# Performance work log

Measured on AMD Instinct MI355X. Metric: run time of the kernel, lower is better.

The kernel has to match this reference:

```python
import jax, jax.numpy as jnp
import numpy as np

N_NODES = 50000


def gcn_conv(x, edge_index, W, b, num_nodes):
    """PyG GCNConv: add self-loops, symmetric norm, gather-scatter aggregate."""
    h = x @ W  # [N, out]
    row = jnp.concatenate([edge_index[0], jnp.arange(num_nodes)])  # sources (+ self loops)
    col = jnp.concatenate([edge_index[1], jnp.arange(num_nodes)])  # targets
    deg = jax.ops.segment_sum(jnp.ones_like(col, dtype=h.dtype), col, num_segments=num_nodes)
    dinv = jnp.where(deg > 0, jax.lax.rsqrt(deg), 0.0)
    norm = dinv[row] * dinv[col]  # [E+N]
    msgs = h[row] * norm[:, None]  # gather + scale
    out = jax.ops.segment_sum(msgs, col, num_segments=num_nodes)  # scatter-add
    return out + b


def setup_inputs() -> dict:
    key = jax.random.key(0)
    ks = jax.random.split(key, 8)
    F_in, H, D = 50, 50, 64
    E_train, Ep, En = 1600000, 200000, 200000
    x = jax.random.normal(ks[0], (N_NODES, F_in), dtype=jnp.float32)
    train_pos_edge_index = jax.random.randint(ks[1], (2, E_train), 0, N_NODES)
    pos_edge_index = jax.random.randint(ks[2], (2, Ep), 0, N_NODES)
    neg_edge_index = jax.random.randint(ks[3], (2, En), 0, N_NODES)
    # Glorot-ish params for the two GCN layers
    W1 = jax.random.normal(ks[4], (F_in, H), dtype=jnp.float32) * (1.0 / np.sqrt(F_in))
    b1 = jnp.zeros((H,), dtype=jnp.float32)
    W2 = jax.random.normal(ks[5], (H, D), dtype=jnp.float32) * (1.0 / np.sqrt(H))
    b2 = jnp.zeros((D,), dtype=jnp.float32)
    return {"x": x, "train_pos_edge_index": train_pos_edge_index,
            "pos_edge_index": pos_edge_index, "neg_edge_index": neg_edge_index,
            "W1": W1, "b1": b1, "W2": W2, "b2": b2}


def reference(x, train_pos_edge_index, pos_edge_index, neg_edge_index, W1, b1, W2, b2):
    # encode: conv1 -> relu -> conv2
    h = gcn_conv(x, train_pos_edge_index, W1, b1, N_NODES)
    h = jax.nn.relu(h)
    z = gcn_conv(h, train_pos_edge_index, W2, b2, N_NODES)  # [N, D]
    # decode: dot product over concatenated pos/neg edge endpoints
    edge_index = jnp.concatenate([pos_edge_index, neg_edge_index], axis=-1)
    logits = jnp.sum(z[edge_index[0]] * z[edge_index[1]], axis=-1)  # [Ep+En]
    return logits
```

## Files before the change

### kernel.cpp

```cpp
#include <hip/hip_runtime.h>
#include <hip/hip_bf16.h>
#include <hip/hip_fp16.h>


constexpr int N_NODES = 50000;
constexpr int NBITS = 6;
constexpr int BNODES = 1 << NBITS;
constexpr int NBUCK = (N_NODES + BNODES - 1) / BNODES;
constexpr int CAP = 2560;
constexpr int CHUNK = 2048;
constexpr int NTILE = 4;
constexpr int TROWS = 12500;

union H4 {
    uint2 u;
    __half2 h[2];
};

__device__ inline float4 h4_to_f4(H4 a) {
    float2 f0 = __half22float2(a.h[0]);
    float2 f1 = __half22float2(a.h[1]);
    return make_float4(f0.x, f0.y, f1.x, f1.y);
}

__device__ inline H4 f4_to_h4(float4 v) {
    H4 r;
    r.h[0] = __floats2half2_rn(v.x, v.y);
    r.h[1] = __floats2half2_rn(v.z, v.w);
    return r;
}

__device__ inline void unpack16(uint4 w0, uint4 w1, int* r) {
    r[0] = (int)(w0.x & 0xffffu);  r[1] = (int)(w0.x >> 16);
    r[2] = (int)(w0.y & 0xffffu);  r[3] = (int)(w0.y >> 16);
    r[4] = (int)(w0.z & 0xffffu);  r[5] = (int)(w0.z >> 16);
    r[6] = (int)(w0.w & 0xffffu);  r[7] = (int)(w0.w >> 16);
    r[8] = (int)(w1.x & 0xffffu);  r[9] = (int)(w1.x >> 16);
    r[10] = (int)(w1.y & 0xffffu); r[11] = (int)(w1.y >> 16);
    r[12] = (int)(w1.z & 0xffffu); r[13] = (int)(w1.z >> 16);
    r[14] = (int)(w1.w & 0xffffu); r[15] = (int)(w1.w >> 16);
}

__global__ __launch_bounds__(256) void partition_kernel(const int4* __restrict__ row4,
                                                        const int4* __restrict__ col4, int E,
                                                        int* __restrict__ cursor,
                                                        unsigned* __restrict__ bEdges) {
    __shared__ unsigned ed[CHUNK];
    __shared__ int cnt[NBUCK];
    __shared__ int base[NBUCK];
    int t = threadIdx.x;
    int e0 = blockIdx.x * CHUNK;
    int n = min(CHUNK, E - e0);
    int n4 = n >> 2;
    for (int i = t; i < NBUCK; i += 256) cnt[i] = 0;
    __syncthreads();
    const int4* r4 = row4 + (e0 >> 2);
    const int4* c4 = col4 + (e0 >> 2);
    for (int i = t; i < n4; i += 256) {
        int4 r = r4[i];
        int4 c = c4[i];
        ed[i * 4 + 0] = ((unsigned)r.x << 16) | (unsigned)c.x;
        ed[i * 4 + 1] = ((unsigned)r.y << 16) | (unsigned)c.y;
        ed[i * 4 + 2] = ((unsigned)r.z << 16) | (unsigned)c.z;
        ed[i * 4 + 3] = ((unsigned)r.w << 16) | (unsigned)c.w;
        atomicAdd(&cnt[c.x >> NBITS], 1);
        atomicAdd(&cnt[c.y >> NBITS], 1);
        atomicAdd(&cnt[c.z >> NBITS], 1);
        atomicAdd(&cnt[c.w >> NBITS], 1);
    }
    __syncthreads();
    for (int i = t; i < NBUCK; i += 256) base[i] = cnt[i] ? atomicAdd(&cursor[i], cnt[i]) : 0;
    __syncthreads();
    for (int i = t; i < NBUCK; i += 256) cnt[i] = 0;
    __syncthreads();
    for (int i = t; i < n; i += 256) {
        unsigned p = ed[i];
        int bk = (int)(p & 0xffffu) >> NBITS;
        int pos = base[bk] + atomicAdd(&cnt[bk], 1);
        if (pos < CAP) bEdges[(size_t)bk * CAP + pos] = p;
    }
}

__global__ __launch_bounds__(256) void bucket_csr_kernel(const int* __restrict__ cursor,
                                                         const unsigned* __restrict__ bEdges,
                                                         unsigned short* __restrict__ srcIdx,
                                                         unsigned* __restrict__ rowmeta,
                                                         float* __restrict__ dinv, int N) {
    __shared__ unsigned ed[CAP];
    __shared__ unsigned short srcL[CAP];
    __shared__ int tdeg[BNODES * NTILE];
    __shared__ int toff[BNODES * NTILE];
    __shared__ int totPad;
    int b = blockIdx.x;
    int tx = threadIdx.x;
    int cnt = min(cursor[b], CAP);
    for (int i = tx; i < BNODES * NTILE; i += 256) tdeg[i] = 0;
    for (int i = tx; i < CAP; i += 256) srcL[i] = 0;
    __syncthreads();
    const unsigned* seg = bEdges + (size_t)b * CAP;
    for (int i = tx; i < cnt; i += 256) {
        unsigned p = seg[i];
        ed[i] = p;
        int l = p & (BNODES - 1);
        int tl = (int)(p >> 16) / TROWS;
        atomicAdd(&tdeg[l * NTILE + tl], 1);
    }
    __syncthreads();
    if (tx < BNODES) {
        int s0 = tdeg[tx * NTILE + 0];
        int s1 = tdeg[tx * NTILE + 1];
        int s2 = tdeg[tx * NTILE + 2];
        int s3 = tdeg[tx * NTILE + 3];
        int d = s0 + s1 + s2 + s3;
        int dpad = (d + 7) & ~7;
        int s = dpad;
#pragma unroll
        for (int off = 1; off < BNODES; off <<= 1) {
            int o = __shfl_up(s, off, 64);
            if (tx >= off) s += o;
        }
        int ex = s - dpad;
        toff[tx * NTILE + 0] = ex;
        toff[tx * NTILE + 1] = ex + s0;
        toff[tx * NTILE + 2] = ex + s0 + s1;
        toff[tx * NTILE + 3] = ex + s0 + s1 + s2;
        if (tx == 63) totPad = min(s, CAP);
        int node = b * BNODES + tx;
        if (node < N) {
            unsigned st = (unsigned)(b * CAP + ex);
            rowmeta[node] = (st << 7) | (unsigned)d;
            dinv[node] = rsqrtf((float)d + 1.0f);
        }
    }
    __syncthreads();
    for (int i = tx; i < BNODES * NTILE; i += 256) tdeg[i] = 0;
    __syncthreads();
    for (int i = tx; i < cnt; i += 256) {
        unsigned p = ed[i];
        int l = p & (BNODES - 1);
        int tl = (int)(p >> 16) / TROWS;
        int pos = toff[l * NTILE + tl] + atomicAdd(&tdeg[l * NTILE + tl], 1);
        srcL[pos] = (unsigned short)(p >> 16);
    }
    __syncthreads();
    int tot = totPad;
    for (int i = tx; i < tot; i += 256) srcIdx[(size_t)b * CAP + i] = srcL[i];
}

template <typename TIN, int K, int INS, int MV>
__global__ __launch_bounds__(256) void matmul_scale_kernel(const TIN* __restrict__ X,
                                                           const float* __restrict__ W,
                                                           const float* __restrict__ dinv,
                                                           uint2* __restrict__ Hs, int N) {
    __shared__ float4 Ws4[K * 16];
    for (int i = threadIdx.x; i < K * 64; i += 256) {
        int k = i >> 6;
        int c = i & 63;
        ((float*)Ws4)[i] = (c < MV) ? W[k * MV + c] : 0.f;
    }
    __syncthreads();
    int tid = blockIdx.x * blockDim.x + threadIdx.x;
    int row = tid >> 4;
    int q = tid & 15;
    if (row >= N) return;
    const TIN* xr = X + (size_t)row * INS;
    float4 acc = make_float4(0.f, 0.f, 0.f, 0.f);
#pragma unroll
    for (int k = 0; k < K; ++k) {
        float xv = (float)xr[k];
        float4 w = Ws4[k * 16 + q];
        acc.x = fmaf(xv, w.x, acc.x);
        acc.y = fmaf(xv, w.y, acc.y);
        acc.z = fmaf(xv, w.z, acc.z);
        acc.w = fmaf(xv, w.w, acc.w);
    }
    float d = dinv[row];
    acc.x *= d;
    acc.y *= d;
    acc.z *= d;
    acc.w *= d;
    Hs[(size_t)row * 16 + q] = f4_to_h4(acc).u;
}

__device__ inline float4 gather_sum(const unsigned short* __restrict__ srcIdx,
                                    const uint2* __restrict__ hs, int node, int q,
                                    unsigned meta) {
    int start = (int)(meta >> 7);
    int d = (int)(meta & 127u);
    int end = start + d;
    H4 t;
    t.u = hs[(size_t)node * 16 + q];
    float4 acc = h4_to_f4(t);
    int j = start;
    while (j + 16 <= end) {
        const uint4* ip = (const uint4*)(srcIdx + j);
        int r[16];
        unpack16(ip[0], ip[1], r);
#pragma unroll
        for (int u = 0; u < 16; ++u) {
            H4 hv;
            hv.u = hs[(size_t)r[u] * 16 + q];
            float4 a = h4_to_f4(hv);
            acc.x += a.x;
            acc.y += a.y;
            acc.z += a.z;
            acc.w += a.w;
        }
        j += 16;
    }
    if (j < end) {
        const uint4* ip = (const uint4*)(srcIdx + j);
        int r[16];
        unpack16(ip[0], ip[1], r);
#pragma unroll
        for (int u = 0; u < 16; ++u) {
            float m = (j + u < end) ? 1.f : 0.f;
            H4 hv;
            hv.u = hs[(size_t)r[u] * 16 + q];
            float4 a = h4_to_f4(hv);
            acc.x = fmaf(m, a.x, acc.x);
            acc.y = fmaf(m, a.y, acc.y);
            acc.z = fmaf(m, a.z, acc.z);
            acc.w = fmaf(m, a.w, acc.w);
        }
    }
    return acc;
}

template <int BC>
__global__ __launch_bounds__(256) void agg_mm_kernel(const unsigned* __restrict__ rowmeta,
                                                     const unsigned short* __restrict__ srcIdx,
                                                     const uint2* __restrict__ hs,
                                                     const float* __restrict__ dinv,
                                                     const float* __restrict__ b1,
                                                     const float* __restrict__ W2,
                                                     uint2* __restrict__ out, int N) {
    __shared__ float4 Ws4[50 * 16];
    __shared__ float h1s[16][68];
    for (int i = threadIdx.x; i < 50 * 64; i += 256) ((float*)Ws4)[i] = W2[i];
    __syncthreads();
    int tid = blockIdx.x * blockDim.x + threadIdx.x;
    int node = tid >> 4;
    int q = tid & 15;
    int g = threadIdx.x >> 4;
    float4 acc = gather_sum(srcIdx, hs, node, q, rowmeta[node]);
    float dv = dinv[node];
    int f = q * 4;
    float4 h1;
    h1.x = fmaxf(dv * acc.x + (f + 0 < BC ? b1[f + 0] : 0.f), 0.f);
    h1.y = fmaxf(dv * acc.y + (f + 1 < BC ? b1[f + 1] : 0.f), 0.f);
    h1.z = fmaxf(dv * acc.z + (f + 2 < BC ? b1[f + 2] : 0.f), 0.f);
    h1.w = fmaxf(dv * acc.w + (f + 3 < BC ? b1[f + 3] : 0.f), 0.f);
    h1s[g][f + 0] = h1.x;
    h1s[g][f + 1] = h1.y;
    h1s[g][f + 2] = h1.z;
    h1s[g][f + 3] = h1.w;
    __syncthreads();
    float4 a2 = make_float4(0.f, 0.f, 0.f, 0.f);
#pragma unroll
    for (int k = 0; k < 50; ++k) {
        float xv = h1s[g][k];
        float4 w = Ws4[k * 16 + q];
        a2.x = fmaf(xv, w.x, a2.x);
        a2.y = fmaf(xv, w.y, a2.y);
        a2.z = fmaf(xv, w.z, a2.z);
        a2.w = fmaf(xv, w.w, a2.w);
    }
    a2.x *= dv;
    a2.y *= dv;
    a2.z *= dv;
    a2.w *= dv;
    out[(size_t)node * 16 + q] = f4_to_h4(a2).u;
}

template <int BC>
__global__ __launch_bounds__(256) void agg_kernel(const unsigned* __restrict__ rowmeta,
                                                  const unsigned short* __restrict__ srcIdx,
                                                  const uint2* __restrict__ hs,
                                                  const float* __restrict__ dinv,
                                                  const float* __restrict__ b,
                                                  uint2* __restrict__ out, int N) {
    int tid = blockIdx.x * blockDim.x + threadIdx.x;
    int node = tid >> 4;
    int q = tid & 15;
    if (node >= N) return;
    float4 acc = gather_sum(srcIdx, hs, node, q, rowmeta[node]);
    float dv = dinv[node];
    int f = q * 4;
    float4 v;
    v.x = dv * acc.x + (f + 0 < BC ? b[f + 0] : 0.f);
    v.y = dv * acc.y + (f + 1 < BC ? b[f + 1] : 0.f);
    v.z = dv * acc.z + (f + 2 < BC ? b[f + 2] : 0.f);
    v.w = dv * acc.w + (f + 3 < BC ? b[f + 3] : 0.f);
    out[(size_t)node * 16 + q] = f4_to_h4(v).u;
}

__global__ __launch_bounds__(256) void decode_kernel(const int* __restrict__ pos,
                                                     const int* __restrict__ neg, int Ep, int En,
                                                     const uint2* __restrict__ z,
                                                     float* __restrict__ logits) {
    int tid = blockIdx.x * blockDim.x + threadIdx.x;
    int e = tid >> 4;
    int q = tid & 15;
    int Etot = Ep + En;
    if (e >= Etot) return;
    int a, bn;
    if (e < Ep) {
        a = pos[e];
        bn = pos[Ep + e];
    } else {
        int t = e - Ep;
        a = neg[t];
        bn = neg[En + t];
    }
    H4 ha, hb;
    ha.u = z[(size_t)a * 16 + q];
    hb.u = z[(size_t)bn * 16 + q];
    float4 za = h4_to_f4(ha);
    float4 zb = h4_to_f4(hb);
    float v = za.x * zb.x + za.y * zb.y + za.z * zb.z + za.w * zb.w;
    v += __shfl_xor(v, 1, 64);
    v += __shfl_xor(v, 2, 64);
    v += __shfl_xor(v, 4, 64);
    v += __shfl_xor(v, 8, 64);
    if (q == 0) logits[e] = v;
}

extern "C" void kernel_launch(void* const* d_in, const int* in_sizes, int n_in,
                              void* d_out, int out_size, void* d_ws, size_t ws_size,
                              hipStream_t stream) {
    const float* x = (const float*)d_in[0];
    const int* train = (const int*)d_in[1];
    const int* pos = (const int*)d_in[2];
    const int* neg = (const int*)d_in[3];
    const float* W1 = (const float*)d_in[4];
    const float* b1 = (const float*)d_in[5];
    const float* W2 = (const float*)d_in[6];
    const float* b2 = (const float*)d_in[7];
    float* logits = (float*)d_out;

    const int FIN = 50;
    const int N = in_sizes[0] / FIN;
    const int E = in_sizes[1] / 2;
    const int Ep = in_sizes[2] / 2;
    const int En = in_sizes[3] / 2;

    const int* t_row = train;
    const int* t_col = train + E;

    float* dinv = (float*)d_ws;
    __half* buf0 = (__half*)(dinv + N);
    __half* buf1 = buf0 + (size_t)N * 64;
    unsigned* rowmeta = (unsigned*)(buf1 + (size_t)N * 64);
    int* cursor = (int*)(rowmeta + N);
    uintptr_t sp = (uintptr_t)(cursor + NBUCK);
    sp = (sp + 15) & ~(uintptr_t)15;
    unsigned short* srcIdx = (unsigned short*)sp;
    unsigned* bEdges = (unsigned*)buf0;

    hipMemsetAsync(cursor, 0, (size_t)NBUCK * sizeof(int), stream);

    partition_kernel<<<(E + CHUNK - 1) / CHUNK, 256, 0, stream>>>((const int4*)t_row,
                                                                  (const int4*)t_col, E, cursor,
                                                                  bEdges);
    bucket_csr_kernel<<<NBUCK, 256, 0, stream>>>(cursor, bEdges, srcIdx, rowmeta, dinv, N);

    const int MMB = (N * 16 + 255) / 256;

    matmul_scale_kernel<float, 50, 50, 50><<<MMB, 256, 0, stream>>>(x, W1, dinv, (uint2*)buf0, N);
    agg_mm_kernel<50><<<MMB, 256, 0, stream>>>(rowmeta, srcIdx, (const uint2*)buf0, dinv, b1, W2,
                                               (uint2*)buf1, N);
    agg_kernel<64><<<MMB, 256, 0, stream>>>(rowmeta, srcIdx, (const uint2*)buf1, dinv, b2,
                                            (uint2*)buf0, N);
    decode_kernel<<<((Ep + En) * 16 + 255) / 256, 256, 0, stream>>>(pos, neg, Ep, En,
                                                                    (const uint2*)buf0, logits);
}
```

Measured before the change: 224.4 us.

## Fuse layer-1 matmul into bucket CSR build and widen decode loads

Folds the first dense matmul (x@W1 scaled by dinv) into the bucket CSR kernel, so each 64-node bucket block stages its x rows and W1 in shared memory and writes Hs directly. This removes one kernel launch and the global re-read of dinv. bEdges moves to its own workspace region instead of aliasing buf0, because buf0 is now written in the same kernel that reads bEdges. The partition chunk size is doubled to 4096, and decode uses 8 lanes with 16-byte loads per edge instead of 16 lanes with 8-byte loads. The trade-off is more shared memory per block, which may lower occupancy, and only NBUCK (~782) blocks are available to do the matmul.

```diff
diff --git a/kernel.cpp b/kernel.cpp
--- a/kernel.cpp
+++ b/kernel.cpp
@@ -8,7 +8,7 @@
 constexpr int BNODES = 1 << NBITS;
 constexpr int NBUCK = (N_NODES + BNODES - 1) / BNODES;
 constexpr int CAP = 2560;
-constexpr int CHUNK = 2048;
+constexpr int CHUNK = 4096;
 constexpr int NTILE = 4;
 constexpr int TROWS = 12500;
 
@@ -39,6 +39,14 @@
     r[10] = (int)(w1.y & 0xffffu); r[11] = (int)(w1.y >> 16);
     r[12] = (int)(w1.z & 0xffffu); r[13] = (int)(w1.z >> 16);
     r[14] = (int)(w1.w & 0xffffu); r[15] = (int)(w1.w >> 16);
+}
+
+__device__ inline float hdot2(unsigned ua, unsigned ub) {
+    __half2 ha = *(__half2*)&ua;
+    __half2 hb = *(__half2*)&ub;
+    float2 fa = __half22float2(ha);
+    float2 fb = __half22float2(hb);
+    return fa.x * fb.x + fa.y * fb.y;
 }
 
 __global__ __launch_bounds__(256) void partition_kernel(const int4* __restrict__ row4,
@@ -81,16 +89,22 @@
     }
 }
 
-__global__ __launch_bounds__(256) void bucket_csr_kernel(const int* __restrict__ cursor,
-                                                         const unsigned* __restrict__ bEdges,
-                                                         unsigned short* __restrict__ srcIdx,
-                                                         unsigned* __restrict__ rowmeta,
-                                                         float* __restrict__ dinv, int N) {
+__global__ __launch_bounds__(256) void bucket_csr_mm_kernel(const int* __restrict__ cursor,
+                                                            const unsigned* __restrict__ bEdges,
+                                                            const float* __restrict__ x,
+                                                            const float* __restrict__ W1,
+                                                            unsigned short* __restrict__ srcIdx,
+                                                            unsigned* __restrict__ rowmeta,
+                                                            float* __restrict__ dinv,
+                                                            uint2* __restrict__ Hs, int N) {
     __shared__ unsigned ed[CAP];
     __shared__ unsigned short srcL[CAP];
     __shared__ int tdeg[BNODES * NTILE];
     __shared__ int toff[BNODES * NTILE];
     __shared__ int totPad;
+    __shared__ float dinvL[BNODES];
+    __shared__ float4 Ws4[50 * 16];
+    __shared__ float xs[BNODES][51];
     int b = blockIdx.x;
     int tx = threadIdx.x;
     int cnt = min(cursor[b], CAP);
@@ -104,6 +118,17 @@
         int l = p & (BNODES - 1);
         int tl = (int)(p >> 16) / TROWS;
         atomicAdd(&tdeg[l * NTILE + tl], 1);
+    }
+    for (int i = tx; i < 50 * 64; i += 256) {
+        int k = i >> 6;
+        int c = i & 63;
+        ((float*)Ws4)[i] = (c < 50) ? W1[k * 50 + c] : 0.f;
+    }
+    for (int i = tx; i < BNODES * 50; i += 256) {
+        int l = i / 50;
+        int k = i - l * 50;
+        int node = b * BNODES + l;
+        xs[l][k] = (node < N) ? x[(size_t)node * 50 + k] : 0.f;
     }
     __syncthreads();
     if (tx < BNODES) {
@@ -125,11 +150,13 @@
         toff[tx * NTILE + 2] = ex + s0 + s1;
         toff[tx * NTILE + 3] = ex + s0 + s1 + s2;
         if (tx == 63) totPad = min(s, CAP);
+        float dvv = rsqrtf((float)d + 1.0f);
+        dinvL[tx] = dvv;
         int node = b * BNODES + tx;
         if (node < N) {
             unsigned st = (unsigned)(b * CAP + ex);
             rowmeta[node] = (st << 7) | (unsigned)d;
-            dinv[node] = rsqrtf((float)d + 1.0f);
+            dinv[node] = dvv;
         }
     }
     __syncthreads();
@@ -145,41 +172,29 @@
     __syncthreads();
     int tot = totPad;
     for (int i = tx; i < tot; i += 256) srcIdx[(size_t)b * CAP + i] = srcL[i];
-}
-
-template <typename TIN, int K, int INS, int MV>
-__global__ __launch_bounds__(256) void matmul_scale_kernel(const TIN* __restrict__ X,
-                                                           const float* __restrict__ W,
-                                                           const float* __restrict__ dinv,
-                                                           uint2* __restrict__ Hs, int N) {
-    __shared__ float4 Ws4[K * 16];
-    for (int i = threadIdx.x; i < K * 64; i += 256) {
-        int k = i >> 6;
-        int c = i & 63;
-        ((float*)Ws4)[i] = (c < MV) ? W[k * MV + c] : 0.f;
-    }
-    __syncthreads();
-    int tid = blockIdx.x * blockDim.x + threadIdx.x;
-    int row = tid >> 4;
-    int q = tid & 15;
-    if (row >= N) return;
-    const TIN* xr = X + (size_t)row * INS;
-    float4 acc = make_float4(0.f, 0.f, 0.f, 0.f);
-#pragma unroll
-    for (int k = 0; k < K; ++k) {
-        float xv = (float)xr[k];
-        float4 w = Ws4[k * 16 + q];
-        acc.x = fmaf(xv, w.x, acc.x);
-        acc.y = fmaf(xv, w.y, acc.y);
-        acc.z = fmaf(xv, w.z, acc.z);
-        acc.w = fmaf(xv, w.w, acc.w);
-    }
-    float d = dinv[row];
-    acc.x *= d;
-    acc.y *= d;
-    acc.z *= d;
-    acc.w *= d;
-    Hs[(size_t)row * 16 + q] = f4_to_h4(acc).u;
+    int q = tx & 15;
+    int g = tx >> 4;
+#pragma unroll
+    for (int rep = 0; rep < 4; ++rep) {
+        int l = g + rep * 16;
+        float4 acc = make_float4(0.f, 0.f, 0.f, 0.f);
+#pragma unroll
+        for (int k = 0; k < 50; ++k) {
+            float xv = xs[l][k];
+            float4 w = Ws4[k * 16 + q];
+            acc.x = fmaf(xv, w.x, acc.x);
+            acc.y = fmaf(xv, w.y, acc.y);
+            acc.z = fmaf(xv, w.z, acc.z);
+            acc.w = fmaf(xv, w.w, acc.w);
+        }
+        float dv = dinvL[l];
+        acc.x *= dv;
+        acc.y *= dv;
+        acc.z *= dv;
+        acc.w *= dv;
+        int node = b * BNODES + l;
+        if (node < N) Hs[(size_t)node * 16 + q] = f4_to_h4(acc).u;
+    }
 }
 
 __device__ inline float4 gather_sum(const unsigned short* __restrict__ srcIdx,
@@ -297,11 +312,11 @@
 
 __global__ __launch_bounds__(256) void decode_kernel(const int* __restrict__ pos,
                                                      const int* __restrict__ neg, int Ep, int En,
-                                                     const uint2* __restrict__ z,
+                                                     const uint4* __restrict__ z4,
                                                      float* __restrict__ logits) {
     int tid = blockIdx.x * blockDim.x + threadIdx.x;
-    int e = tid >> 4;
-    int q = tid & 15;
+    int e = tid >> 3;
+    int q = tid & 7;
     int Etot = Ep + En;
     if (e >= Etot) return;
     int a, bn;
@@ -313,16 +328,12 @@
         a = neg[t];
         bn = neg[En + t];
     }
-    H4 ha, hb;
-    ha.u = z[(size_t)a * 16 + q];
-    hb.u = z[(size_t)bn * 16 + q];
-    float4 za = h4_to_f4(ha);
-    float4 zb = h4_to_f4(hb);
-    float v = za.x * zb.x + za.y * zb.y + za.z * zb.z + za.w * zb.w;
+    uint4 ua = z4[(size_t)a * 8 + q];
+    uint4 ub = z4[(size_t)bn * 8 + q];
+    float v = hdot2(ua.x, ub.x) + hdot2(ua.y, ub.y) + hdot2(ua.z, ub.z) + hdot2(ua.w, ub.w);
     v += __shfl_xor(v, 1, 64);
     v += __shfl_xor(v, 2, 64);
     v += __shfl_xor(v, 4, 64);
-    v += __shfl_xor(v, 8, 64);
     if (q == 0) logits[e] = v;
 }
 
@@ -356,22 +367,24 @@
     uintptr_t sp = (uintptr_t)(cursor + NBUCK);
     sp = (sp + 15) & ~(uintptr_t)15;
     unsigned short* srcIdx = (unsigned short*)sp;
-    unsigned* bEdges = (unsigned*)buf0;
+    uintptr_t bp = (uintptr_t)(srcIdx + (size_t)NBUCK * CAP);
+    bp = (bp + 15) & ~(uintptr_t)15;
+    unsigned* bEdges = (unsigned*)bp;
 
     hipMemsetAsync(cursor, 0, (size_t)NBUCK * sizeof(int), stream);
 
     partition_kernel<<<(E + CHUNK - 1) / CHUNK, 256, 0, stream>>>((const int4*)t_row,
                                                                   (const int4*)t_col, E, cursor,
                                                                   bEdges);
-    bucket_csr_kernel<<<NBUCK, 256, 0, stream>>>(cursor, bEdges, srcIdx, rowmeta, dinv, N);
+    bucket_csr_mm_kernel<<<NBUCK, 256, 0, stream>>>(cursor, bEdges, x, W1, srcIdx, rowmeta, dinv,
+                                                    (uint2*)buf0, N);
 
     const int MMB = (N * 16 + 255) / 256;
 
-    matmul_scale_kernel<float, 50, 50, 50><<<MMB, 256, 0, stream>>>(x, W1, dinv, (uint2*)buf0, N);
     agg_mm_kernel<50><<<MMB, 256, 0, stream>>>(rowmeta, srcIdx, (const uint2*)buf0, dinv, b1, W2,
                                                (uint2*)buf1, N);
     agg_kernel<64><<<MMB, 256, 0, stream>>>(rowmeta, srcIdx, (const uint2*)buf1, dinv, b2,
                                             (uint2*)buf0, N);
-    decode_kernel<<<((Ep + En) * 16 + 255) / 256, 256, 0, stream>>>(pos, neg, Ep, En,
-                                                                    (const uint2*)buf0, logits);
-}
+    decode_kernel<<<((Ep + En) * 8 + 255) / 256, 256, 0, stream>>>(pos, neg, Ep, En,
+                                                                   (const uint4*)buf0, logits);
+}
```

Result: faster. 217.5 us (-3.1%).
